# Kernel optimization log

Measured on AMD Instinct MI355X. Metric: run time of the kernel, lower is better.

The kernel has to match this reference:

```python
import jax, jax.numpy as jnp
import numpy as np

B, S, D, P, NQ = 8, 2048, 1024, 256, 8192


def setup_inputs() -> dict:
    key = jax.random.key(0)
    ks = jax.random.split(key, 8)
    return {
        "flag": 0,
        "encoded_input": jax.random.normal(ks[0], (B, S, D), dtype=jnp.float32),
        "start_ids_1": jax.random.randint(ks[1], (NQ,), 0, S, dtype=jnp.int32),
        "end_ids_1": jax.random.randint(ks[2], (NQ,), 0, S, dtype=jnp.int32),
        "query_batch_idx": jax.random.randint(ks[3], (NQ,), 0, B, dtype=jnp.int32),
        "start_ids_2": jax.random.randint(ks[4], (NQ,), 0, S, dtype=jnp.int32),
        "end_ids_2": jax.random.randint(ks[5], (NQ,), 0, S, dtype=jnp.int32),
        "W": jax.random.normal(ks[6], (D, P), dtype=jnp.float32) * 0.02,
        "b": jnp.zeros((P,), dtype=jnp.float32),
    }


def _gather_spans(h, qb, s, e):
    # span_repr[b, i, j] = concat(h[b, i], h[b, j]) for j >= i, else 0.
    # Direct gather instead of building the O(seq^2) table.
    rep = jnp.concatenate([h[qb, s], h[qb, e]], axis=-1)  # [NQ, 2*P]
    valid = (e >= s).astype(rep.dtype)[:, None]
    return rep * valid


def reference(flag, encoded_input, start_ids_1, end_ids_1, query_batch_idx,
              start_ids_2, end_ids_2, W, b):
    h = encoded_input @ W + b  # [B, S, P] (use_proj=True)
    res1 = _gather_spans(h, query_batch_idx, start_ids_1, end_ids_1)
    res2 = _gather_spans(h, query_batch_idx, start_ids_2, end_ids_2)
    return (res1, res2)
```

## Files before the change

### kernel.cpp

```cpp
#include <hip/hip_runtime.h>
#include <hip/hip_bf16.h>
#include <stdint.h>

#define S_LEN 2048
#define D_DIM 1024
#define P_DIM 256
#define NQ_   8192
#define M_TOT 16384
#define CAP 32
#define HS  260

typedef __attribute__((ext_vector_type(4))) float  f32x4;
typedef __attribute__((ext_vector_type(8))) __bf16 bf16x8;


__global__ __launch_bounds__(1024) void wtf_kernel(const float* __restrict__ W,
                                                   __bf16* __restrict__ WTf,
                                                   int* __restrict__ cnt) {
    __shared__ float tile[32][33];
    const int bx = blockIdx.x;
    const int by = blockIdx.y;
    const int k0 = bx * 32, n0 = by * 32;
    const int tx = threadIdx.x, ty = threadIdx.y;
    const int g = (by * 32 + bx) * 1024 + ty * 32 + tx;
    if (g < M_TOT) cnt[g] = 0;
    tile[ty][tx] = W[(k0 + ty) * P_DIM + (n0 + tx)];
    __syncthreads();
    const int t = ty * 32 + tx;
    if (t < 128) {
        const int c16r = t >> 6, q = (t >> 4) & 3, lm = t & 15;
        bf16x8 v;
        #pragma unroll
        for (int e = 0; e < 8; ++e) v[e] = (__bf16)tile[q * 8 + e][c16r * 16 + lm];
        const int c16 = by * 2 + c16r;
        const int ts  = bx >> 1, kh = bx & 1;
        *(bf16x8*)(WTf + (size_t)((c16 * 32 + ts * 2 + kh) * 512 + (q * 16 + lm) * 8)) = v;
    }
}

__global__ __launch_bounds__(256) void a_cvt(const float* __restrict__ A,
                                             __bf16* __restrict__ Af) {
    const int b  = blockIdx.x;
    const int t  = threadIdx.x;
    const int rr = t >> 4;
    const int cq = t & 15;
    const float* src = A  + (size_t)(b * 16 + rr) * D_DIM;
    __bf16*      dst = Af + (size_t)b * 16384;
    #pragma unroll
    for (int it = 0; it < 8; ++it) {
        const int c = it * 16 + cq;
        const float4 x0 = *(const float4*)(src + c * 8);
        const float4 x1 = *(const float4*)(src + c * 8 + 4);
        bf16x8 v;
        v[0] = (__bf16)x0.x; v[1] = (__bf16)x0.y; v[2] = (__bf16)x0.z; v[3] = (__bf16)x0.w;
        v[4] = (__bf16)x1.x; v[5] = (__bf16)x1.y; v[6] = (__bf16)x1.z; v[7] = (__bf16)x1.w;
        const int ts = c >> 3, kh = (c >> 2) & 1, qp = c & 3;
        *(bf16x8*)(dst + (ts * 2 + kh) * 512 + (qp * 16 + rr) * 8) = v;
    }
}

__global__ __launch_bounds__(256) void index_zero(const int* __restrict__ s1,
                                                  const int* __restrict__ e1,
                                                  const int* __restrict__ s2,
                                                  const int* __restrict__ e2,
                                                  const int* __restrict__ qb,
                                                  int* __restrict__ cnt,
                                                  int* __restrict__ bucket,
                                                  float* __restrict__ out) {
    const int q    = blockIdx.x * 256 + threadIdx.x;
    const int lane = threadIdx.x & 63;
    const int bqw  = blockIdx.x * 256 + (threadIdx.x & ~63);
    const int b    = qb[q];
    const float4 z = make_float4(0.f, 0.f, 0.f, 0.f);
    #pragma unroll
    for (int set = 0; set < 2; ++set) {
        const int s = set ? s2[q] : s1[q];
        const int e = set ? e2[q] : e1[q];
        if (e >= s) {
            int r = b * S_LEN + s;
            int k = atomicAdd(&cnt[r], 1); if (k < CAP) bucket[r * CAP + k] = (q << 2) | (set << 1);
            r = b * S_LEN + e;
            k = atomicAdd(&cnt[r], 1);     if (k < CAP) bucket[r * CAP + k] = (q << 2) | (set << 1) | 1;
        }
        unsigned long long mask = __ballot(e < s);
        while (mask) {
            const int j = __ffsll(mask) - 1;
            mask &= mask - 1;
            const int qz = bqw + j;
            float4* dst = (float4*)(out + (size_t)set * (NQ_ * 512) + (size_t)qz * 512);
            dst[lane]      = z;
            dst[lane + 64] = z;
        }
    }
}

__global__ __launch_bounds__(256, 2) void gemm_kernel(const __bf16* __restrict__ Af,
                                                      const __bf16* __restrict__ WTf,
                                                      const float*  __restrict__ bias,
                                                      const int*    __restrict__ cnt,
                                                      const int*    __restrict__ bucket,
                                                      float*        __restrict__ out) {
    __shared__ float hs[32 * HS];
    __shared__ int s_cnt[32];
    __shared__ int s_off[33];
    __shared__ int elist[32 * CAP];

    const int tid = threadIdx.x;
    const int w   = tid >> 6;
    const int l   = tid & 63;
    const int lm  = l & 15;
    const int q   = l >> 4;

    const int m0  = blockIdx.x * 32;
    const int r16 = blockIdx.x * 2;

    const __bf16* apb[2][2];
    const __bf16* bpb[4][2];
    #pragma unroll
    for (int mi = 0; mi < 2; ++mi)
        #pragma unroll
        for (int kh = 0; kh < 2; ++kh)
            apb[mi][kh] = Af + (size_t)(((r16 + mi) * 32 + kh) * 512 + l * 8);
    #pragma unroll
    for (int ni = 0; ni < 4; ++ni)
        #pragma unroll
        for (int kh = 0; kh < 2; ++kh)
            bpb[ni][kh] = WTf + (size_t)(((w * 4 + ni) * 32 + kh) * 512 + l * 8);

    bf16x8 a_[2][2][2];
    bf16x8 b_[2][4][2];
    f32x4  acc[2][4] = {};

#define LOADSTEP(B, T)                                                        \
    _Pragma("unroll") for (int mi = 0; mi < 2; ++mi)                          \
        _Pragma("unroll") for (int kh = 0; kh < 2; ++kh)                      \
            a_[B][mi][kh] = *(const bf16x8*)(apb[mi][kh] + (T) * 1024);       \
    _Pragma("unroll") for (int ni = 0; ni < 4; ++ni)                          \
        _Pragma("unroll") for (int kh = 0; kh < 2; ++kh)                      \
            b_[B][ni][kh] = *(const bf16x8*)(bpb[ni][kh] + (T) * 1024);

#define MMASTEP(B)                                                            \
    _Pragma("unroll") for (int kh = 0; kh < 2; ++kh)                          \
        _Pragma("unroll") for (int mi = 0; mi < 2; ++mi)                      \
            _Pragma("unroll") for (int ni = 0; ni < 4; ++ni)                  \
                acc[mi][ni] = __builtin_amdgcn_mfma_f32_16x16x32_bf16(        \
                    a_[B][mi][kh], b_[B][ni][kh], acc[mi][ni], 0, 0, 0);

    LOADSTEP(0, 0)
    #pragma unroll 1
    for (int t = 0; t < 14; t += 2) {
        LOADSTEP(1, t + 1)
        MMASTEP(0)
        LOADSTEP(0, t + 2)
        MMASTEP(1)
    }
    LOADSTEP(1, 15)
    MMASTEP(0)
    MMASTEP(1)
#undef LOADSTEP
#undef MMASTEP

    if (tid < 32) { int c = cnt[m0 + tid]; s_cnt[tid] = c < CAP ? c : CAP; }

    #pragma unroll
    for (int ni = 0; ni < 4; ++ni) {
        const int col = w * 64 + ni * 16 + lm;
        const float bv = bias[col];
        #pragma unroll
        for (int mi = 0; mi < 2; ++mi) {
            const int rbase = mi * 16 + q * 4;
            #pragma unroll
            for (int r = 0; r < 4; ++r)
                hs[(rbase + r) * HS + col] = acc[mi][ni][r] + bv;
        }
    }
    __syncthreads();
    if (tid == 0) {
        int a = 0;
        #pragma unroll 1
        for (int i = 0; i < 32; ++i) { s_off[i] = a; a += s_cnt[i]; }
        s_off[32] = a;
    }
    __syncthreads();
    if (tid < 32) {
        const int o = s_off[tid], c = s_cnt[tid];
        const int* bk = bucket + (size_t)(m0 + tid) * CAP;
        for (int k = 0; k < c; ++k)
            elist[o + k] = (tid << 15) | (bk[k] & 0x7fff);
    }
    __syncthreads();

    const int E   = s_off[32];
    const int grp = tid >> 6;
    const int gl  = tid & 63;
    #pragma unroll 1
    for (int j = grp; j < E; j += 4) {
        const int ent  = elist[j];
        const int rl   = ent >> 15;
        const int code = ent & 0x7fff;
        const int qq   = code >> 2;
        const int st   = (code >> 1) & 1;
        const int hf   = code & 1;
        const float4 v = *(const float4*)&hs[rl * HS + gl * 4];
        *(float4*)(out + (size_t)st * (NQ_ * 512) + (size_t)qq * 512 + hf * 256 + gl * 4) = v;
    }
}

extern "C" void kernel_launch(void* const* d_in, const int* in_sizes, int n_in,
                              void* d_out, int out_size, void* d_ws, size_t ws_size,
                              hipStream_t stream) {
    const float* A    = (const float*)d_in[1];
    const int*   s1   = (const int*)  d_in[2];
    const int*   e1   = (const int*)  d_in[3];
    const int*   qb   = (const int*)  d_in[4];
    const int*   s2   = (const int*)  d_in[5];
    const int*   e2   = (const int*)  d_in[6];
    const float* W    = (const float*)d_in[7];
    const float* bias = (const float*)d_in[8];
    float*       out  = (float*)d_out;

    __bf16* WTf    = (__bf16*)d_ws;
    int*    cnt    = (int*)((char*)d_ws + (1 << 20));
    int*    bucket = (int*)((char*)d_ws + (1 << 20) + (1 << 16));
    __bf16* Af     = (__bf16*)((char*)d_ws + (16 << 20));

    a_cvt      <<<dim3(1024), dim3(256), 0, stream>>>(A, Af);
    wtf_kernel <<<dim3(32, 8), dim3(32, 32), 0, stream>>>(W, WTf, cnt);
    index_zero <<<dim3(NQ_ / 256), dim3(256), 0, stream>>>(s1, e1, s2, e2, qb, cnt, bucket, out);
    gemm_kernel<<<dim3(M_TOT / 32), dim3(256), 0, stream>>>(Af, WTf, bias, cnt, bucket, out);
}
```

Baseline: 154.1 us.

## Fuse fp32-to-bf16 A conversion into GEMM via swizzled LDS staging

```diff
diff --git a/kernel.cpp b/kernel.cpp
--- a/kernel.cpp
+++ b/kernel.cpp
@@ -38,27 +38,6 @@
     }
 }
 
-__global__ __launch_bounds__(256) void a_cvt(const float* __restrict__ A,
-                                             __bf16* __restrict__ Af) {
-    const int b  = blockIdx.x;
-    const int t  = threadIdx.x;
-    const int rr = t >> 4;
-    const int cq = t & 15;
-    const float* src = A  + (size_t)(b * 16 + rr) * D_DIM;
-    __bf16*      dst = Af + (size_t)b * 16384;
-    #pragma unroll
-    for (int it = 0; it < 8; ++it) {
-        const int c = it * 16 + cq;
-        const float4 x0 = *(const float4*)(src + c * 8);
-        const float4 x1 = *(const float4*)(src + c * 8 + 4);
-        bf16x8 v;
-        v[0] = (__bf16)x0.x; v[1] = (__bf16)x0.y; v[2] = (__bf16)x0.z; v[3] = (__bf16)x0.w;
-        v[4] = (__bf16)x1.x; v[5] = (__bf16)x1.y; v[6] = (__bf16)x1.z; v[7] = (__bf16)x1.w;
-        const int ts = c >> 3, kh = (c >> 2) & 1, qp = c & 3;
-        *(bf16x8*)(dst + (ts * 2 + kh) * 512 + (qp * 16 + rr) * 8) = v;
-    }
-}
-
 __global__ __launch_bounds__(256) void index_zero(const int* __restrict__ s1,
                                                   const int* __restrict__ e1,
                                                   const int* __restrict__ s2,
@@ -67,40 +46,37 @@
                                                   int* __restrict__ cnt,
                                                   int* __restrict__ bucket,
                                                   float* __restrict__ out) {
-    const int q    = blockIdx.x * 256 + threadIdx.x;
     const int lane = threadIdx.x & 63;
-    const int bqw  = blockIdx.x * 256 + (threadIdx.x & ~63);
+    const int q    = blockIdx.x * 64 + lane;
+    const int set  = threadIdx.x >> 7;
+    const int half = (threadIdx.x >> 6) & 1;
     const int b    = qb[q];
+    const int s = set ? s2[q] : s1[q];
+    const int e = set ? e2[q] : e1[q];
+    if (!half && e >= s) {
+        int r = b * S_LEN + s;
+        int k = atomicAdd(&cnt[r], 1); if (k < CAP) bucket[r * CAP + k] = (q << 2) | (set << 1);
+        r = b * S_LEN + e;
+        k = atomicAdd(&cnt[r], 1);     if (k < CAP) bucket[r * CAP + k] = (q << 2) | (set << 1) | 1;
+    }
+    unsigned long long mask = __ballot(e < s);
+    const int bqw = blockIdx.x * 64;
     const float4 z = make_float4(0.f, 0.f, 0.f, 0.f);
-    #pragma unroll
-    for (int set = 0; set < 2; ++set) {
-        const int s = set ? s2[q] : s1[q];
-        const int e = set ? e2[q] : e1[q];
-        if (e >= s) {
-            int r = b * S_LEN + s;
-            int k = atomicAdd(&cnt[r], 1); if (k < CAP) bucket[r * CAP + k] = (q << 2) | (set << 1);
-            r = b * S_LEN + e;
-            k = atomicAdd(&cnt[r], 1);     if (k < CAP) bucket[r * CAP + k] = (q << 2) | (set << 1) | 1;
-        }
-        unsigned long long mask = __ballot(e < s);
-        while (mask) {
-            const int j = __ffsll(mask) - 1;
-            mask &= mask - 1;
-            const int qz = bqw + j;
-            float4* dst = (float4*)(out + (size_t)set * (NQ_ * 512) + (size_t)qz * 512);
-            dst[lane]      = z;
-            dst[lane + 64] = z;
-        }
-    }
-}
-
-__global__ __launch_bounds__(256, 2) void gemm_kernel(const __bf16* __restrict__ Af,
+    while (mask) {
+        const int j = __ffsll(mask) - 1;
+        mask &= mask - 1;
+        float* dst = out + (size_t)set * (NQ_ * 512) + (size_t)(bqw + j) * 512 + half * 256;
+        ((float4*)dst)[lane] = z;
+    }
+}
+
+__global__ __launch_bounds__(256, 2) void gemm_kernel(const float*  __restrict__ A,
                                                       const __bf16* __restrict__ WTf,
                                                       const float*  __restrict__ bias,
                                                       const int*    __restrict__ cnt,
                                                       const int*    __restrict__ bucket,
                                                       float*        __restrict__ out) {
-    __shared__ float hs[32 * HS];
+    __shared__ __align__(16) __bf16 Afl[32768];
     __shared__ int s_cnt[32];
     __shared__ int s_off[33];
     __shared__ int elist[32 * CAP];
@@ -111,54 +87,72 @@
     const int lm  = l & 15;
     const int q   = l >> 4;
 
-    const int m0  = blockIdx.x * 32;
-    const int r16 = blockIdx.x * 2;
-
-    const __bf16* apb[2][2];
-    const __bf16* bpb[4][2];
-    #pragma unroll
-    for (int mi = 0; mi < 2; ++mi)
-        #pragma unroll
-        for (int kh = 0; kh < 2; ++kh)
-            apb[mi][kh] = Af + (size_t)(((r16 + mi) * 32 + kh) * 512 + l * 8);
+    const int m0 = blockIdx.x * 32;
+    const int ph = (blockIdx.x * 5) & 15;
+
+    {
+        const int r   = tid >> 3;
+        const int la  = tid & 7;
+        const int mi  = r >> 4, lmr = r & 15;
+        const float* src = A + (size_t)(m0 + r) * D_DIM;
+        #pragma unroll
+        for (int it = 0; it < 16; ++it) {
+            const int c = it * 8 + la;
+            const float4 x0 = *(const float4*)(src + c * 8);
+            const float4 x1 = *(const float4*)(src + c * 8 + 4);
+            bf16x8 v;
+            v[0] = (__bf16)x0.x; v[1] = (__bf16)x0.y; v[2] = (__bf16)x0.z; v[3] = (__bf16)x0.w;
+            v[4] = (__bf16)x1.x; v[5] = (__bf16)x1.y; v[6] = (__bf16)x1.z; v[7] = (__bf16)x1.w;
+            const int kt = c >> 3, kh = (c >> 2) & 1, qp = c & 3;
+            const int slot = lmr ^ (qp << 1);
+            *(bf16x8*)(&Afl[(mi * 32 + kt * 2 + kh) * 512 + qp * 128 + slot * 8]) = v;
+        }
+    }
+    __syncthreads();
+
+    const int slotr = lm ^ (q << 1);
+    const __bf16* abase = Afl + q * 128 + slotr * 8;
+    const __bf16* bp[4][2];
     #pragma unroll
     for (int ni = 0; ni < 4; ++ni)
         #pragma unroll
         for (int kh = 0; kh < 2; ++kh)
-            bpb[ni][kh] = WTf + (size_t)(((w * 4 + ni) * 32 + kh) * 512 + l * 8);
-
-    bf16x8 a_[2][2][2];
-    bf16x8 b_[2][4][2];
+            bp[ni][kh] = WTf + (size_t)(((w * 4 + ni) * 32 + kh) * 512 + l * 8);
+
+    bf16x8 bre[3][4][2];
     f32x4  acc[2][4] = {};
 
-#define LOADSTEP(B, T)                                                        \
-    _Pragma("unroll") for (int mi = 0; mi < 2; ++mi)                          \
-        _Pragma("unroll") for (int kh = 0; kh < 2; ++kh)                      \
-            a_[B][mi][kh] = *(const bf16x8*)(apb[mi][kh] + (T) * 1024);       \
+#define LOADB(B, T) {                                                         \
+    const int kt_ = ((T) + ph) & 15;                                          \
     _Pragma("unroll") for (int ni = 0; ni < 4; ++ni)                          \
         _Pragma("unroll") for (int kh = 0; kh < 2; ++kh)                      \
-            b_[B][ni][kh] = *(const bf16x8*)(bpb[ni][kh] + (T) * 1024);
-
-#define MMASTEP(B)                                                            \
-    _Pragma("unroll") for (int kh = 0; kh < 2; ++kh)                          \
-        _Pragma("unroll") for (int mi = 0; mi < 2; ++mi)                      \
-            _Pragma("unroll") for (int ni = 0; ni < 4; ++ni)                  \
-                acc[mi][ni] = __builtin_amdgcn_mfma_f32_16x16x32_bf16(        \
-                    a_[B][mi][kh], b_[B][ni][kh], acc[mi][ni], 0, 0, 0);
-
-    LOADSTEP(0, 0)
-    #pragma unroll 1
-    for (int t = 0; t < 14; t += 2) {
-        LOADSTEP(1, t + 1)
-        MMASTEP(0)
-        LOADSTEP(0, t + 2)
-        MMASTEP(1)
-    }
-    LOADSTEP(1, 15)
-    MMASTEP(0)
-    MMASTEP(1)
-#undef LOADSTEP
-#undef MMASTEP
+            bre[B][ni][kh] = *(const bf16x8*)(bp[ni][kh] + kt_ * 1024); }
+
+    LOADB(0, 0)
+    LOADB(1, 1)
+    #pragma unroll
+    for (int t = 0; t < 16; ++t) {
+        if (t < 14) LOADB((t + 2) % 3, t + 2)
+        const int kt_ = (t + ph) & 15;
+        bf16x8 af[2][2];
+        #pragma unroll
+        for (int mi = 0; mi < 2; ++mi)
+            #pragma unroll
+            for (int kh = 0; kh < 2; ++kh)
+                af[mi][kh] = *(const bf16x8*)(abase + (mi * 32 + kt_ * 2 + kh) * 512);
+        #pragma unroll
+        for (int kh = 0; kh < 2; ++kh)
+            #pragma unroll
+            for (int mi = 0; mi < 2; ++mi)
+                #pragma unroll
+                for (int ni = 0; ni < 4; ++ni)
+                    acc[mi][ni] = __builtin_amdgcn_mfma_f32_16x16x32_bf16(
+                        af[mi][kh], bre[t % 3][ni][kh], acc[mi][ni], 0, 0, 0);
+    }
+#undef LOADB
+
+    __syncthreads();
+    float* hs = (float*)Afl;
 
     if (tid < 32) { int c = cnt[m0 + tid]; s_cnt[tid] = c < CAP ? c : CAP; }
 
@@ -222,10 +216,8 @@
     __bf16* WTf    = (__bf16*)d_ws;
     int*    cnt    = (int*)((char*)d_ws + (1 << 20));
     int*    bucket = (int*)((char*)d_ws + (1 << 20) + (1 << 16));
-    __bf16* Af     = (__bf16*)((char*)d_ws + (16 << 20));
-
-    a_cvt      <<<dim3(1024), dim3(256), 0, stream>>>(A, Af);
+
     wtf_kernel <<<dim3(32, 8), dim3(32, 32), 0, stream>>>(W, WTf, cnt);
-    index_zero <<<dim3(NQ_ / 256), dim3(256), 0, stream>>>(s1, e1, s2, e2, qb, cnt, bucket, out);
-    gemm_kernel<<<dim3(M_TOT / 32), dim3(256), 0, stream>>>(Af, WTf, bias, cnt, bucket, out);
-}
+    index_zero <<<dim3(NQ_ / 64), dim3(256), 0, stream>>>(s1, e1, s2, e2, qb, cnt, bucket, out);
+    gemm_kernel<<<dim3(M_TOT / 32), dim3(256), 0, stream>>>(A, WTf, bias, cnt, bucket, out);
+}
```

Result: faster. 135.9 us (-11.8%).
